# Performance work log

Measured on AMD Instinct MI355X. Metric: run time of the kernel, lower is better.

## Reference

```python
import jax, jax.numpy as jnp
import numpy as np

N = 100000  # num nodes
E = 1600000  # num edges
D_IN = 64
D_OUT = 64


def setup_inputs() -> dict:
    key = jax.random.key(0)
    k = jax.random.split(key, 8)
    x = jax.random.normal(k[0], (N, D_IN), dtype=jnp.float32)
    edge_index = jax.random.randint(k[1], (2, E), 0, N, dtype=jnp.int64)
    s1 = 1.0 / np.sqrt(D_IN)
    s2 = 1.0 / np.sqrt(D_OUT)
    W1 = jax.random.uniform(k[2], (D_IN, D_OUT), jnp.float32, -s1, s1)
    b1 = jax.random.uniform(k[3], (D_OUT,), jnp.float32, -s1, s1)
    W2 = jax.random.uniform(k[4], (D_OUT, D_OUT), jnp.float32, -s2, s2)
    b2 = jax.random.uniform(k[5], (D_OUT,), jnp.float32, -s2, s2)
    eps = jnp.asarray(0.0, dtype=jnp.float32)  # learnable (train_eps=True)
    return {"x": x, "edge_index": edge_index, "W1": W1, "b1": b1, "W2": W2, "b2": b2, "eps": eps}


def reference(x, edge_index, W1, b1, W2, b2, eps):
    src, dst = edge_index[0], edge_index[1]
    # sum-aggregate neighbor features: agg[i] = sum_{(j->i)} x[j]
    agg = jax.ops.segment_sum(x[src], dst, num_segments=N)  # [N, D_IN]
    h = (1.0 + eps) * x + agg
    h = jax.nn.relu(h @ W1 + b1)
    return h @ W2 + b2
```

## Files before the change

### kernel.cpp

```cpp
#include <hip/hip_runtime.h>

#define NN 100000
#define NE 1600000
#define D  64
#define NPB 196
#define NBK 512
#define RPL 8
#define CAPR 512
#define CHUNK 2048
#define EPT (CHUNK / 256)
#define NCH ((NE + CHUNK - 1) / CHUNK)
#define CVTB ((NN * D / 16 + 255) / 256)
#define WSTR 72


typedef unsigned short u16;
typedef __attribute__((ext_vector_type(8))) short bf16x8;
typedef __attribute__((ext_vector_type(4))) float f32x4;

__device__ __forceinline__ u16 f32_to_bf16_rn(float f) {
    unsigned u = __float_as_uint(f);
    return (u16)((u + 0x7FFF + ((u >> 16) & 1)) >> 16);
}
__device__ __forceinline__ unsigned pk2(float lo, float hi) {
    return (unsigned)f32_to_bf16_rn(lo) | ((unsigned)f32_to_bf16_rn(hi) << 16);
}
__device__ __forceinline__ float bf16_to_f32(u16 h) {
    return __uint_as_float(((unsigned)h) << 16);
}

__global__ __launch_bounds__(256) void bin_cvt_kernel(const float* __restrict__ x,
                                                      u16* __restrict__ xb,
                                                      const int* __restrict__ ei,
                                                      int* __restrict__ cursor,
                                                      int* __restrict__ bins) {
    __shared__ int lc[NBK];
    __shared__ int lbase[NBK];
    const int t = threadIdx.x;

    if (blockIdx.x >= NCH) {
        int i = ((blockIdx.x - NCH) * 256 + t) * 16;
        if (i < NN * D) {
            float4 a = *(const float4*)(x + i);
            float4 b = *(const float4*)(x + i + 4);
            float4 c = *(const float4*)(x + i + 8);
            float4 d = *(const float4*)(x + i + 12);
            uint4 o1, o2;
            o1.x = pk2(a.x, a.y); o1.y = pk2(a.z, a.w);
            o1.z = pk2(b.x, b.y); o1.w = pk2(b.z, b.w);
            o2.x = pk2(c.x, c.y); o2.y = pk2(c.z, c.w);
            o2.z = pk2(d.x, d.y); o2.w = pk2(d.z, d.w);
            *(uint4*)(xb + i) = o1;
            *(uint4*)(xb + i + 8) = o2;
        }
        return;
    }

    const int base = blockIdx.x * CHUNK;
    const int rep  = blockIdx.x & (RPL - 1);

    int dsts[EPT];
    #pragma unroll
    for (int j = 0; j < EPT; ++j) {
        int e = base + t + j * 256;
        dsts[j] = (e < NE) ? ei[NE + e] : -1;
    }

    for (int i = t; i < NBK; i += 256) lc[i] = 0;
    __syncthreads();
    #pragma unroll
    for (int j = 0; j < EPT; ++j)
        if (dsts[j] >= 0) atomicAdd(&lc[(unsigned)dsts[j] / NPB], 1);
    __syncthreads();
    for (int i = t; i < NBK; i += 256) {
        int c = lc[i];
        lbase[i] = c ? atomicAdd(&cursor[rep * NBK + i], c) : 0;
        lc[i] = 0;
    }
    __syncthreads();
    #pragma unroll
    for (int j = 0; j < EPT; ++j) {
        if (dsts[j] >= 0) {
            int src = ei[base + t + j * 256];
            int dst = dsts[j];
            int b   = (unsigned)dst / NPB;
            int loc = dst - b * NPB;
            int o   = atomicAdd(&lc[b], 1);
            int pos = lbase[b] + o;
            if (pos < CAPR)
                bins[(b * RPL + rep) * CAPR + pos] = (loc << 17) | src;
        }
    }
}

__global__ __launch_bounds__(1024) void agg_kernel(const u16* __restrict__ xb,
                                                   const float* __restrict__ eps,
                                                   const int* __restrict__ cursor,
                                                   const int* __restrict__ bins,
                                                   u16* __restrict__ hb) {
    __shared__ int sorted[RPL * CAPR];
    __shared__ int tmp[256];
    __shared__ int off[257];
    __shared__ int cur[256];
    __shared__ int wsum[4];
    const int b    = blockIdx.x;
    const int t    = threadIdx.x;
    const int lane = t & 63;
    const int w    = t >> 6;
    const float e1 = 1.0f + *eps;

    if (t < 256) tmp[t] = 0;
    int vals[RPL];
    #pragma unroll
    for (int r = 0; r < RPL; ++r) {
        int n = min(cursor[r * NBK + b], CAPR);
        vals[r] = (t < n) ? bins[(b * RPL + r) * CAPR + t] : -1;
    }
    __syncthreads();
    #pragma unroll
    for (int r = 0; r < RPL; ++r)
        if (vals[r] >= 0) atomicAdd(&tmp[vals[r] >> 17], 1);
    __syncthreads();
    if (t < 256) {
        int v = tmp[t];
        int inc = v;
        #pragma unroll
        for (int s = 1; s < 64; s <<= 1) {
            int u = __shfl_up(inc, s);
            if (lane >= s) inc += u;
        }
        if (lane == 63) wsum[w] = inc;
        __syncthreads();
        int pre = 0;
        #pragma unroll
        for (int k = 0; k < 4; ++k) pre += (k < w) ? wsum[k] : 0;
        off[t] = pre + inc - v;
        cur[t] = pre + inc - v;
        if (t == 255) off[256] = pre + inc;
    } else {
        __syncthreads();
    }
    __syncthreads();
    #pragma unroll
    for (int r = 0; r < RPL; ++r) {
        if (vals[r] >= 0) {
            int pos = atomicAdd(&cur[vals[r] >> 17], 1);
            sorted[pos] = vals[r] & 0x1FFFF;
        }
    }
    __syncthreads();

    #pragma unroll
    for (int j = 0; j < 13; ++j) {
        int r = w + 16 * j;
        if (r < NPB) {
            int node = b * NPB + r;
            if (node < NN) {
                float a = e1 * bf16_to_f32(xb[node * D + lane]);
                int p  = off[r];
                int pe = off[r + 1];
                for (; p + 8 <= pe; p += 8) {
                    int i0 = sorted[p],     i1 = sorted[p + 1];
                    int i2 = sorted[p + 2], i3 = sorted[p + 3];
                    int i4 = sorted[p + 4], i5 = sorted[p + 5];
                    int i6 = sorted[p + 6], i7 = sorted[p + 7];
                    float v0 = bf16_to_f32(xb[i0 * D + lane]);
                    float v1 = bf16_to_f32(xb[i1 * D + lane]);
                    float v2 = bf16_to_f32(xb[i2 * D + lane]);
                    float v3 = bf16_to_f32(xb[i3 * D + lane]);
                    float v4 = bf16_to_f32(xb[i4 * D + lane]);
                    float v5 = bf16_to_f32(xb[i5 * D + lane]);
                    float v6 = bf16_to_f32(xb[i6 * D + lane]);
                    float v7 = bf16_to_f32(xb[i7 * D + lane]);
                    a += ((v0 + v1) + (v2 + v3)) + ((v4 + v5) + (v6 + v7));
                }
                for (; p + 4 <= pe; p += 4) {
                    int i0 = sorted[p],     i1 = sorted[p + 1];
                    int i2 = sorted[p + 2], i3 = sorted[p + 3];
                    float v0 = bf16_to_f32(xb[i0 * D + lane]);
                    float v1 = bf16_to_f32(xb[i1 * D + lane]);
                    float v2 = bf16_to_f32(xb[i2 * D + lane]);
                    float v3 = bf16_to_f32(xb[i3 * D + lane]);
                    a += (v0 + v1) + (v2 + v3);
                }
                for (; p < pe; ++p) a += bf16_to_f32(xb[sorted[p] * D + lane]);
                hb[node * D + lane] = f32_to_bf16_rn(a);
            }
        }
    }
}

__global__ __launch_bounds__(256, 2) void mlp_mfma_kernel(
        const u16* __restrict__ hb, float* __restrict__ out,
        const float* __restrict__ W1, const float* __restrict__ b1,
        const float* __restrict__ W2, const float* __restrict__ b2) {
    __shared__ u16 wt1[D * WSTR];
    __shared__ u16 wt2[D * WSTR];
    __shared__ u16 lds[4][16 * WSTR];
    const int lane = threadIdx.x & 63;
    const int wv   = threadIdx.x >> 6;
    const int m    = lane & 15;
    const int q    = lane >> 4;
    u16* tile = &lds[wv][0];

    for (int i = threadIdx.x; i < D * D; i += 256) {
        int k = i >> 6, n = i & 63;
        wt1[n * WSTR + k] = f32_to_bf16_rn(W1[i]);
        wt2[n * WSTR + k] = f32_to_bf16_rn(W2[i]);
    }
    __syncthreads();

    bf16x8 wb1[4][2], wb2[4][2];
    #pragma unroll
    for (int t = 0; t < 4; ++t)
        #pragma unroll
        for (int s = 0; s < 2; ++s) {
            const int o = (t * 16 + m) * WSTR + s * 32 + q * 8;
            wb1[t][s] = *(const bf16x8*)&wt1[o];
            wb2[t][s] = *(const bf16x8*)&wt2[o];
        }
    float bias1[4], bias2[4];
    #pragma unroll
    for (int t = 0; t < 4; ++t) {
        bias1[t] = b1[t * 16 + m];
        bias2[t] = b2[t * 16 + m];
    }

    const int wave = blockIdx.x * 4 + wv;
    const int nw   = gridDim.x * 4;
    for (int ti = wave; ti < NN / 16; ti += nw) {
        const int rowbase = ti * 16;

        bf16x8 a1f[2];
        #pragma unroll
        for (int s = 0; s < 2; ++s)
            a1f[s] = *(const bf16x8*)(hb + (rowbase + m) * D + s * 32 + q * 8);

        #pragma unroll
        for (int t = 0; t < 4; ++t) {
            f32x4 cc = {0.f, 0.f, 0.f, 0.f};
            cc = __builtin_amdgcn_mfma_f32_16x16x32_bf16(a1f[0], wb1[t][0], cc, 0, 0, 0);
            cc = __builtin_amdgcn_mfma_f32_16x16x32_bf16(a1f[1], wb1[t][1], cc, 0, 0, 0);
            #pragma unroll
            for (int r = 0; r < 4; ++r) {
                float vv = fmaxf(cc[r] + bias1[t], 0.0f);
                tile[(q * 4 + r) * WSTR + t * 16 + m] = f32_to_bf16_rn(vv);
            }
        }

        bf16x8 a2f[2];
        #pragma unroll
        for (int s = 0; s < 2; ++s)
            a2f[s] = *(const bf16x8*)&tile[m * WSTR + s * 32 + q * 8];

        #pragma unroll
        for (int t = 0; t < 4; ++t) {
            f32x4 cc = {0.f, 0.f, 0.f, 0.f};
            cc = __builtin_amdgcn_mfma_f32_16x16x32_bf16(a2f[0], wb2[t][0], cc, 0, 0, 0);
            cc = __builtin_amdgcn_mfma_f32_16x16x32_bf16(a2f[1], wb2[t][1], cc, 0, 0, 0);
            #pragma unroll
            for (int r = 0; r < 4; ++r)
                out[(rowbase + q * 4 + r) * D + t * 16 + m] = cc[r] + bias2[t];
        }
    }
}

extern "C" void kernel_launch(void* const* d_in, const int* in_sizes, int n_in,
                              void* d_out, int out_size, void* d_ws, size_t ws_size,
                              hipStream_t stream) {
    const float* x   = (const float*)d_in[0];
    const int*   ei  = (const int*)d_in[1];
    const float* W1  = (const float*)d_in[2];
    const float* b1  = (const float*)d_in[3];
    const float* W2  = (const float*)d_in[4];
    const float* b2  = (const float*)d_in[5];
    const float* eps = (const float*)d_in[6];
    float*       out = (float*)d_out;

    int* cursor = (int*)d_ws;
    int* bins   = cursor + RPL * NBK;
    u16* xb     = (u16*)(bins + NBK * RPL * CAPR);
    u16* hb     = xb + NN * D;

    hipMemsetAsync(cursor, 0, RPL * NBK * sizeof(int), stream);
    bin_cvt_kernel<<<NCH + CVTB, 256, 0, stream>>>(x, xb, ei, cursor, bins);
    agg_kernel<<<NBK, 1024, 0, stream>>>(xb, eps, cursor, bins, hb);
    mlp_mfma_kernel<<<512, 256, 0, stream>>>(hb, out, W1, b1, W2, b2);
}
```

Baseline: 149.0 us.

## Locally sort edges per bucket in LDS before coalesced bin writes

Raises the edge chunk per block from 2048 to 8192. Edges are first counting-sorted by bucket in shared memory using a wave-shuffle prefix scan, then each wave copies whole bucket runs to global bins with lane-contiguous stores. This replaces scattered single-word global writes with mostly contiguous ones and cuts global cursor atomics per edge. In exchange it adds extra LDS use (about 40KB), more syncs, a serial per-bucket copy loop, and fewer blocks (about 196 binning blocks), which lowers parallelism.

New measurement: 176.7 us. +18.6%, slower.

```diff
diff --git a/kernel.cpp b/kernel.cpp
--- a/kernel.cpp
+++ b/kernel.cpp
@@ -7,7 +7,7 @@
 #define NBK 512
 #define RPL 8
 #define CAPR 512
-#define CHUNK 2048
+#define CHUNK 8192
 #define EPT (CHUNK / 256)
 #define NCH ((NE + CHUNK - 1) / CHUNK)
 #define CVTB ((NN * D / 16 + 255) / 256)
@@ -35,7 +35,11 @@
                                                       int* __restrict__ cursor,
                                                       int* __restrict__ bins) {
     __shared__ int lc[NBK];
+    __shared__ int ls[NBK];
     __shared__ int lbase[NBK];
+    __shared__ int lcur[NBK];
+    __shared__ int wsum[4];
+    __shared__ int lbuf[CHUNK];
     const int t = threadIdx.x;
 
     if (blockIdx.x >= NCH) {
@@ -58,6 +62,8 @@
 
     const int base = blockIdx.x * CHUNK;
     const int rep  = blockIdx.x & (RPL - 1);
+    const int lane = t & 63;
+    const int w    = t >> 6;
 
     int dsts[EPT];
     #pragma unroll
@@ -66,18 +72,33 @@
         dsts[j] = (e < NE) ? ei[NE + e] : -1;
     }
 
-    for (int i = t; i < NBK; i += 256) lc[i] = 0;
+    lc[t] = 0; lc[t + 256] = 0;
     __syncthreads();
     #pragma unroll
     for (int j = 0; j < EPT; ++j)
         if (dsts[j] >= 0) atomicAdd(&lc[(unsigned)dsts[j] / NPB], 1);
     __syncthreads();
-    for (int i = t; i < NBK; i += 256) {
-        int c = lc[i];
-        lbase[i] = c ? atomicAdd(&cursor[rep * NBK + i], c) : 0;
-        lc[i] = 0;
-    }
-    __syncthreads();
+
+    int c0 = lc[2 * t], c1 = lc[2 * t + 1];
+    int s  = c0 + c1;
+    int inc = s;
+    #pragma unroll
+    for (int st = 1; st < 64; st <<= 1) {
+        int u = __shfl_up(inc, st);
+        if (lane >= st) inc += u;
+    }
+    if (lane == 63) wsum[w] = inc;
+    lbase[2 * t]     = c0 ? atomicAdd(&cursor[rep * NBK + 2 * t], c0) : 0;
+    lbase[2 * t + 1] = c1 ? atomicAdd(&cursor[rep * NBK + 2 * t + 1], c1) : 0;
+    __syncthreads();
+    int pre = 0;
+    #pragma unroll
+    for (int k = 0; k < 4; ++k) pre += (k < w) ? wsum[k] : 0;
+    int ex = pre + inc - s;
+    ls[2 * t] = ex;         ls[2 * t + 1] = ex + c0;
+    lcur[2 * t] = ex;       lcur[2 * t + 1] = ex + c0;
+    __syncthreads();
+
     #pragma unroll
     for (int j = 0; j < EPT; ++j) {
         if (dsts[j] >= 0) {
@@ -85,10 +106,25 @@
             int dst = dsts[j];
             int b   = (unsigned)dst / NPB;
             int loc = dst - b * NPB;
-            int o   = atomicAdd(&lc[b], 1);
-            int pos = lbase[b] + o;
-            if (pos < CAPR)
-                bins[(b * RPL + rep) * CAPR + pos] = (loc << 17) | src;
+            int o   = atomicAdd(&lcur[b], 1);
+            lbuf[o] = (loc << 17) | src;
+        }
+    }
+    __syncthreads();
+
+    for (int it = 0; it < NBK / 4; ++it) {
+        int b    = it * 4 + w;
+        int cnt  = lc[b];
+        int lsrc = ls[b];
+        int gdst = (b * RPL + rep) * CAPR;
+        int gb   = lbase[b];
+        for (int o = 0; o < cnt; o += 64) {
+            int k = o + lane;
+            if (k < cnt) {
+                int pos = gb + k;
+                if (pos < CAPR)
+                    bins[gdst + pos] = lbuf[lsrc + k];
+            }
         }
     }
 }
```
